# Kernel tuning notes

Hardware: AMD Instinct MI355X
Metric: run time of the kernel (lower is better)

The kernel has to match this reference:

```python
import jax, jax.numpy as jnp
import numpy as np

B, E, K = 2048, 16, 4
D_SF, D_OF, D_PPF, D_PVF = 512, 512, 256, 256
D = D_SF + D_OF + D_PPF + D_PVF  # 1536 = moe_input_size
H = 1024
N_OBJ, N_PRED = 36, 132
EPS = float(np.finfo(np.float64).eps)  # matches np.finfo(float).eps in combine
NOISE_EPS = 1e-2


def setup_inputs() -> dict:
    key = jax.random.key(0)
    ks = jax.random.split(key, 12)
    r = lambda i, shape, scale=1.0: (jax.random.normal(ks[i], shape, jnp.float32) * scale)
    return {
        "sf": r(0, (B, D_SF)),
        "of": r(1, (B, D_OF)),
        "ppf": r(2, (B, D_PPF)),
        "pvf": r(3, (B, D_PVF)),
        "w_gate": r(4, (D, E), 0.02),
        "w_noise": r(5, (D, E), 0.02),
        "W1": r(6, (E, D, H), 1.0 / np.sqrt(D)),
        "b1": jnp.zeros((E, H), jnp.float32),
        "W2": r(7, (E, H, H), 1.0 / np.sqrt(H)),
        "b2": jnp.zeros((E, H), jnp.float32),
        "Ws": r(8, (E, H, N_OBJ), 1.0 / np.sqrt(H)),
        "bs": jnp.zeros((E, N_OBJ), jnp.float32),
        "Wo": r(9, (E, H, N_OBJ), 1.0 / np.sqrt(H)),
        "bo": jnp.zeros((E, N_OBJ), jnp.float32),
        "Wp": r(10, (E, H, N_PRED), 1.0 / np.sqrt(H)),
        "bp": jnp.zeros((E, N_PRED), jnp.float32),
        "noise": r(11, (B, E)),
    }


def _noisy_top_k_gates(x, w_gate, w_noise, noise):
    """Shazeer noisy top-k gating -> sparse [B, E] gate matrix."""
    clean_logits = x @ w_gate                                   # [B, E]
    noise_stddev = jax.nn.softplus(x @ w_noise) + NOISE_EPS      # [B, E]
    logits = clean_logits + noise * noise_stddev
    top_vals, top_idx = jax.lax.top_k(logits, K)                 # [B, K]
    top_gates = jax.nn.softmax(top_vals, axis=-1)                # renormalized over top-k
    gates = jnp.zeros_like(logits)
    gates = gates.at[jnp.arange(x.shape[0])[:, None], top_idx].set(top_gates)
    return gates


def _combine(log_scores, gates):
    """SparseDispatcher.combine_expert_output, dense-equivalent.
    log_scores: [E, B, C] per-expert log-probs; gates: [B, E].
    output[b] = log(sum_e gates[b,e] * exp(log_scores[e,b])), eps where all-zero.
    gates==0 exactly zeroes the non-routed experts (same as sparse index_add).
    """
    w = gates.T[:, :, None]                                      # [E, B, 1]
    combined = jnp.sum(jnp.exp(log_scores) * w, axis=0)          # [B, C]
    combined = jnp.where(combined == 0, EPS, combined)
    return jnp.log(combined)


def reference(sf, of, ppf, pvf, w_gate, w_noise,
              W1, b1, W2, b2, Ws, bs, Wo, bo, Wp, bp, noise):
    x = jnp.concatenate([sf, of, ppf, pvf], axis=-1)             # [B, D]
    gates = _noisy_top_k_gates(x, w_gate, w_noise, noise)        # [B, E]

    # All-expert dense evaluation (grouped GEMM): 3-layer relu MLP trunk.
    h1 = jax.nn.relu(jnp.einsum('bd,edh->ebh', x, W1) + b1[:, None, :])   # [E, B, H]
    h2 = jax.nn.relu(jnp.einsum('ebh,ehg->ebg', h1, W2) + b2[:, None, :])  # [E, B, H]

    s_log = jax.nn.log_softmax(jnp.einsum('ebh,ehc->ebc', h2, Ws) + bs[:, None, :], axis=-1)
    o_log = jax.nn.log_softmax(jnp.einsum('ebh,ehc->ebc', h2, Wo) + bo[:, None, :], axis=-1)
    p_log = jax.nn.log_softmax(jnp.einsum('ebh,ehc->ebc', h2, Wp) + bp[:, None, :], axis=-1)

    s_out = _combine(s_log, gates)   # [B, N_OBJ]
    o_out = _combine(o_log, gates)   # [B, N_OBJ]
    p_out = _combine(p_log, gates)   # [B, N_PRED]
    return s_out, o_out, p_out
```

## Files before the change

kernel.cpp:

```cpp
#include <hip/hip_runtime.h>
#include <hip/hip_bf16.h>
#include <cstdint>

typedef __attribute__((ext_vector_type(8))) short short8;
typedef __attribute__((ext_vector_type(4))) float f32x4;

constexpr int B_ = 2048, E_ = 16, D_ = 1536, H_ = 1024;
constexpr int NHEAD = 256;
constexpr float EPS_ = 2.220446049250313e-16f;

__device__ __forceinline__ void gload_lds16(const void* g, void* l) {
  __builtin_amdgcn_global_load_lds((const __attribute__((address_space(1))) void*)g,
                                   (__attribute__((address_space(3))) void*)l,
                                   16, 0, 0);
}

__global__ __launch_bounds__(256) void pack_x(
    const float* __restrict__ sf, const float* __restrict__ of_,
    const float* __restrict__ ppf, const float* __restrict__ pvf,
    __hip_bfloat16* __restrict__ xb)
{
  const int b = blockIdx.x;
  for (int d = threadIdx.x; d < D_; d += 256) {
    float v;
    if (d < 512)       v = sf[b * 512 + d];
    else if (d < 1024) v = of_[b * 512 + (d - 512)];
    else if (d < 1280) v = ppf[b * 256 + (d - 1024)];
    else               v = pvf[b * 256 + (d - 1280)];
    xb[(size_t)b * D_ + d] = __float2bfloat16(v);
  }
}

__global__ __launch_bounds__(256) void gate_kernel(
    const float* __restrict__ sf, const float* __restrict__ of_,
    const float* __restrict__ ppf, const float* __restrict__ pvf,
    const float* __restrict__ wg, const float* __restrict__ wn,
    const float* __restrict__ noise,
    int* __restrict__ topidx, float* __restrict__ topw)
{
  __shared__ float xs[D_];
  __shared__ float sums[32];
  const int b = blockIdx.x, t = threadIdx.x;
  for (int d = t; d < D_; d += 256) {
    float v;
    if (d < 512)       v = sf[b * 512 + d];
    else if (d < 1024) v = of_[b * 512 + (d - 512)];
    else if (d < 1280) v = ppf[b * 256 + (d - 1024)];
    else               v = pvf[b * 256 + (d - 1280)];
    xs[d] = v;
  }
  __syncthreads();
  const int job = t >> 3, sub = t & 7;
  const int e = job & 15;
  const float* w = (job < 16) ? wg : wn;
  float p = 0.f;
  for (int d = sub; d < D_; d += 8) p += xs[d] * w[d * 16 + e];
  p += __shfl_down(p, 4, 8);
  p += __shfl_down(p, 2, 8);
  p += __shfl_down(p, 1, 8);
  if (sub == 0) sums[job] = p;
  __syncthreads();
  if (t == 0) {
    float lg[16];
    for (int i = 0; i < 16; ++i) {
      float z = sums[16 + i];
      float sp = (z > 0.f) ? (z + log1pf(expf(-z))) : log1pf(expf(z));
      lg[i] = sums[i] + noise[b * 16 + i] * (sp + 1e-2f);
    }
    float tv[4]; int ti[4];
    unsigned used = 0;
    for (int k = 0; k < 4; ++k) {
      float best = -INFINITY; int bi = 0;
      for (int i = 0; i < 16; ++i)
        if (!((used >> i) & 1u) && lg[i] > best) { best = lg[i]; bi = i; }
      used |= 1u << bi; tv[k] = best; ti[k] = bi;
    }
    float s = 0.f, ex[4];
    for (int k = 0; k < 4; ++k) { ex[k] = expf(tv[k] - tv[0]); s += ex[k]; }
    for (int k = 0; k < 4; ++k) { topw[b * 4 + k] = ex[k] / s; topidx[b * 4 + k] = ti[k]; }
  }
}

__global__ __launch_bounds__(256) void transpose_bf16(
    const float* __restrict__ src, __hip_bfloat16* __restrict__ dst, int K, int N)
{
  __shared__ float tile[32][33];
  const int e = blockIdx.z;
  const int n0 = blockIdx.x * 32, k0 = blockIdx.y * 32;
  const int tx = threadIdx.x, ty = threadIdx.y;
  const float* s = src + (size_t)e * K * N;
  __hip_bfloat16* d = dst + (size_t)e * N * K;
#pragma unroll
  for (int r = 0; r < 4; ++r) {
    const int k = k0 + ty + r * 8;
    tile[ty + r * 8][tx] = s[(size_t)k * N + n0 + tx];
  }
  __syncthreads();
#pragma unroll
  for (int r = 0; r < 4; ++r) {
    const int n = n0 + ty + r * 8;
    d[(size_t)n * K + k0 + tx] = __float2bfloat16(tile[tx][ty + r * 8]);
  }
}

__global__ __launch_bounds__(256) void head_transpose(
    const float* __restrict__ Wsp, const float* __restrict__ Wop,
    const float* __restrict__ Wpp, __hip_bfloat16* __restrict__ dst)
{
  __shared__ float tile[32][33];
  const int e = blockIdx.z;
  const int k0 = blockIdx.x * 32;
  const int n0 = blockIdx.y * 32;
  const int tx = threadIdx.x, ty = threadIdx.y;
#pragma unroll
  for (int r = 0; r < 4; ++r) {
    const int k = k0 + ty + r * 8;
    const int n = n0 + tx;
    float v;
    if (n < 36)       v = Wsp[((size_t)e * H_ + k) * 36 + n];
    else if (n < 72)  v = Wop[((size_t)e * H_ + k) * 36 + (n - 36)];
    else if (n < 204) v = Wpp[((size_t)e * H_ + k) * 132 + (n - 72)];
    else              v = 0.f;
    tile[ty + r * 8][tx] = v;
  }
  __syncthreads();
#pragma unroll
  for (int r = 0; r < 4; ++r) {
    const int n = n0 + ty + r * 8;
    dst[((size_t)e * NHEAD + n) * H_ + k0 + tx] = __float2bfloat16(tile[tx][ty + r * 8]);
  }
}

__global__ __launch_bounds__(256) void pack_hbias(
    const float* __restrict__ bs, const float* __restrict__ bo,
    const float* __restrict__ bp, float* __restrict__ hb)
{
  const int e = blockIdx.x, t = threadIdx.x;
  float v = 0.f;
  if (t < 36)       v = bs[e * 36 + t];
  else if (t < 72)  v = bo[e * 36 + (t - 36)];
  else if (t < 204) v = bp[e * 132 + (t - 72)];
  hb[e * NHEAD + t] = v;
}

template <int EPI>
__global__ __launch_bounds__(256) void gemm_bt(
    const __hip_bfloat16* __restrict__ A, size_t strideA, int ldA,
    const __hip_bfloat16* __restrict__ Bm, size_t strideB,
    const float* __restrict__ bias,
    void* __restrict__ Cout, size_t strideC, int ldC,
    int K)
{
  __shared__ __align__(16) __hip_bfloat16 lA[128 * 64];
  __shared__ __align__(16) __hip_bfloat16 lB[128 * 64];
  const int e = blockIdx.z;
  const int bm = blockIdx.x, bn = blockIdx.y;
  const int t = threadIdx.x;
  const int w = t >> 6, lane = t & 63;
  const int wm = w >> 1, wn = w & 1;
  const __hip_bfloat16* Ae = A + (size_t)e * strideA + (size_t)(bm * 128) * ldA;
  const __hip_bfloat16* Be = Bm + (size_t)e * strideB + (size_t)(bn * 128) * K;
  const int rsub = lane >> 3;
  const int csub = (lane & 7) * 8;

  f32x4 acc[4][4];
#pragma unroll
  for (int m = 0; m < 4; ++m)
#pragma unroll
    for (int n = 0; n < 4; ++n) acc[m][n] = (f32x4){0.f, 0.f, 0.f, 0.f};

  const int KT = K >> 6;
  const int arow = wm * 64 + (lane & 15);
  const int brow = wn * 64 + (lane & 15);
  const int khalf = (lane >> 4) * 8;

  for (int kt = 0; kt < KT; ++kt) {
    const int k0 = kt << 6;
    __syncthreads();
#pragma unroll
    for (int j = 0; j < 4; ++j) {
      const int r = j * 32 + w * 8 + rsub;
      gload_lds16(Ae + (size_t)r * ldA + (k0 + csub), &lA[j * 2048 + w * 512]);
      gload_lds16(Be + (size_t)r * K + (k0 + csub), &lB[j * 2048 + w * 512]);
    }
    asm volatile("s_waitcnt vmcnt(0)" ::: "memory");
    __syncthreads();
#pragma unroll
    for (int kk = 0; kk < 2; ++kk) {
      short8 af[4], bfr[4];
#pragma unroll
      for (int m = 0; m < 4; ++m)
        af[m] = *(const short8*)&lA[(arow + m * 16) * 64 + kk * 32 + khalf];
#pragma unroll
      for (int n = 0; n < 4; ++n)
        bfr[n] = *(const short8*)&lB[(brow + n * 16) * 64 + kk * 32 + khalf];
#pragma unroll
      for (int m = 0; m < 4; ++m)
#pragma unroll
        for (int n = 0; n < 4; ++n)
          acc[m][n] = __builtin_amdgcn_mfma_f32_16x16x32_bf16(af[m], bfr[n], acc[m][n], 0, 0, 0);
    }
  }

  const int rbase = (lane >> 4) * 4, cbase = lane & 15;
#pragma unroll
  for (int n = 0; n < 4; ++n) {
    const int gcol = bn * 128 + wn * 64 + n * 16 + cbase;
    const float bv = bias[(size_t)e * ldC + gcol];
#pragma unroll
    for (int m = 0; m < 4; ++m) {
      const int grow = bm * 128 + wm * 64 + m * 16 + rbase;
#pragma unroll
      for (int j = 0; j < 4; ++j) {
        float v = acc[m][n][j] + bv;
        const size_t idx = (size_t)e * strideC + (size_t)(grow + j) * ldC + gcol;
        if (EPI == 0) {
          ((__hip_bfloat16*)Cout)[idx] = __float2bfloat16(v > 0.f ? v : 0.f);
        } else {
          ((float*)Cout)[idx] = v;
        }
      }
    }
  }
}

__global__ __launch_bounds__(256) void combine_kernel(
    const float* __restrict__ logits, const int* __restrict__ topidx,
    const float* __restrict__ topw, float* __restrict__ out)
{
  __shared__ float rows[4][204];
  __shared__ float lse[4][3];
  __shared__ float wk[4];
  const int b = blockIdx.x, t = threadIdx.x;
  if (t < 4) wk[t] = topw[b * 4 + t];
#pragma unroll
  for (int k = 0; k < 4; ++k) {
    const int e = topidx[b * 4 + k];
    if (t < 204) rows[k][t] = logits[((size_t)e * B_ + b) * NHEAD + t];
  }
  __syncthreads();
  const int wv = t >> 6, lane = t & 63;
  const int segbase[3] = {0, 36, 72};
  const int segcnt[3] = {36, 36, 132};
  for (int s = 0; s < 3; ++s) {
    float mx = -INFINITY;
    for (int c = lane; c < segcnt[s]; c += 64) mx = fmaxf(mx, rows[wv][segbase[s] + c]);
    for (int o = 32; o > 0; o >>= 1) mx = fmaxf(mx, __shfl_xor(mx, o));
    float sum = 0.f;
    for (int c = lane; c < segcnt[s]; c += 64) sum += expf(rows[wv][segbase[s] + c] - mx);
    for (int o = 32; o > 0; o >>= 1) sum += __shfl_xor(sum, o);
    if (lane == 0) lse[wv][s] = mx + logf(sum);
  }
  __syncthreads();
  if (t < 204) {
    const int seg = t < 36 ? 0 : (t < 72 ? 1 : 2);
    float acc = 0.f;
    for (int k = 0; k < 4; ++k) acc += wk[k] * expf(rows[k][t] - lse[k][seg]);
    if (acc == 0.f) acc = EPS_;
    const float r = logf(acc);
    if (t < 36)      out[b * 36 + t] = r;
    else if (t < 72) out[73728 + b * 36 + (t - 36)] = r;
    else             out[147456 + b * 132 + (t - 72)] = r;
  }
}

extern "C" void kernel_launch(void* const* d_in, const int* in_sizes, int n_in,
                              void* d_out, int out_size, void* d_ws, size_t ws_size,
                              hipStream_t stream)
{
  (void)in_sizes; (void)n_in; (void)out_size; (void)ws_size;
  const float* sf      = (const float*)d_in[0];
  const float* of_     = (const float*)d_in[1];
  const float* ppf     = (const float*)d_in[2];
  const float* pvf     = (const float*)d_in[3];
  const float* w_gate  = (const float*)d_in[4];
  const float* w_noise = (const float*)d_in[5];
  const float* W1      = (const float*)d_in[6];
  const float* b1      = (const float*)d_in[7];
  const float* W2      = (const float*)d_in[8];
  const float* b2      = (const float*)d_in[9];
  const float* Ws      = (const float*)d_in[10];
  const float* bs      = (const float*)d_in[11];
  const float* Wo      = (const float*)d_in[12];
  const float* bo      = (const float*)d_in[13];
  const float* Wp      = (const float*)d_in[14];
  const float* bp      = (const float*)d_in[15];
  const float* noise   = (const float*)d_in[16];

  char* ws = (char*)d_ws;
  size_t off = 0;
  auto take = [&](size_t bytes) -> void* {
    void* p = ws + off; off += (bytes + 255) & ~(size_t)255; return p;
  };
  __hip_bfloat16* xb  = (__hip_bfloat16*)take((size_t)B_ * D_ * 2);
  __hip_bfloat16* W1T = (__hip_bfloat16*)take((size_t)E_ * H_ * D_ * 2);
  __hip_bfloat16* W2T = (__hip_bfloat16*)take((size_t)E_ * H_ * H_ * 2);
  __hip_bfloat16* WhT = (__hip_bfloat16*)take((size_t)E_ * NHEAD * H_ * 2);
  float* hbias        = (float*)take((size_t)E_ * NHEAD * 4);
  __hip_bfloat16* h1  = (__hip_bfloat16*)take((size_t)E_ * B_ * H_ * 2);
  __hip_bfloat16* h2  = (__hip_bfloat16*)take((size_t)E_ * B_ * H_ * 2);
  int* topidx         = (int*)take((size_t)B_ * 4 * 4);
  float* topw         = (float*)take((size_t)B_ * 4 * 4);
  float* logits       = (float*)h1;

  pack_x<<<B_, 256, 0, stream>>>(sf, of_, ppf, pvf, xb);
  gate_kernel<<<B_, 256, 0, stream>>>(sf, of_, ppf, pvf, w_gate, w_noise, noise, topidx, topw);
  transpose_bf16<<<dim3(H_ / 32, D_ / 32, E_), dim3(32, 8), 0, stream>>>(W1, W1T, D_, H_);
  transpose_bf16<<<dim3(H_ / 32, H_ / 32, E_), dim3(32, 8), 0, stream>>>(W2, W2T, H_, H_);
  head_transpose<<<dim3(H_ / 32, NHEAD / 32, E_), dim3(32, 8), 0, stream>>>(Ws, Wo, Wp, WhT);
  pack_hbias<<<E_, 256, 0, stream>>>(bs, bo, bp, hbias);

  gemm_bt<0><<<dim3(B_ / 128, H_ / 128, E_), 256, 0, stream>>>(
      xb, 0, D_, W1T, (size_t)H_ * D_, b1, h1, (size_t)B_ * H_, H_, D_);
  gemm_bt<0><<<dim3(B_ / 128, H_ / 128, E_), 256, 0, stream>>>(
      h1, (size_t)B_ * H_, H_, W2T, (size_t)H_ * H_, b2, h2, (size_t)B_ * H_, H_, H_);
  gemm_bt<1><<<dim3(B_ / 128, NHEAD / 128, E_), 256, 0, stream>>>(
      h2, (size_t)B_ * H_, H_, WhT, (size_t)NHEAD * H_, hbias, logits, (size_t)B_ * NHEAD, NHEAD, H_);

  combine_kernel<<<B_, 256, 0, stream>>>(logits, topidx, topw, (float*)d_out);
}
```

Baseline: 661.0 us.

## Route tokens to top-k experts and run sparse grouped GEMMs

Replaces dense all-expert evaluation with MoE-style routing. The gate kernel counts tokens per expert, a schedule kernel builds per-expert 128-row tiles, rows are gathered into a packed buffer, and the three GEMMs run only over routed rows via a tile table. This cuts GEMM work to the top-4 of 16 experts. In exchange it adds several small serial kernels and atomics, and it caps the schedule at 80 tiles, which could drop rows if the expert distribution is skewed.

```diff
diff --git a/kernel.cpp b/kernel.cpp
--- a/kernel.cpp
+++ b/kernel.cpp
@@ -7,6 +7,8 @@
 
 constexpr int B_ = 2048, E_ = 16, D_ = 1536, H_ = 1024;
 constexpr int NHEAD = 256;
+constexpr int TOTROWS = B_ * 4;
+constexpr int MAXTILES = 80;
 constexpr float EPS_ = 2.220446049250313e-16f;
 
 __device__ __forceinline__ void gload_lds16(const void* g, void* l) {
@@ -15,20 +17,8 @@
                                    16, 0, 0);
 }
 
-__global__ __launch_bounds__(256) void pack_x(
-    const float* __restrict__ sf, const float* __restrict__ of_,
-    const float* __restrict__ ppf, const float* __restrict__ pvf,
-    __hip_bfloat16* __restrict__ xb)
-{
-  const int b = blockIdx.x;
-  for (int d = threadIdx.x; d < D_; d += 256) {
-    float v;
-    if (d < 512)       v = sf[b * 512 + d];
-    else if (d < 1024) v = of_[b * 512 + (d - 512)];
-    else if (d < 1280) v = ppf[b * 256 + (d - 1024)];
-    else               v = pvf[b * 256 + (d - 1280)];
-    xb[(size_t)b * D_ + d] = __float2bfloat16(v);
-  }
+__global__ __launch_bounds__(64) void zero_small(int* __restrict__ p, int n) {
+  if ((int)threadIdx.x < n) p[threadIdx.x] = 0;
 }
 
 __global__ __launch_bounds__(256) void gate_kernel(
@@ -36,7 +26,7 @@
     const float* __restrict__ ppf, const float* __restrict__ pvf,
     const float* __restrict__ wg, const float* __restrict__ wn,
     const float* __restrict__ noise,
-    int* __restrict__ topidx, float* __restrict__ topw)
+    int* __restrict__ topidx, float* __restrict__ topw, int* __restrict__ counts)
 {
   __shared__ float xs[D_];
   __shared__ float sums[32];
@@ -77,7 +67,69 @@
     }
     float s = 0.f, ex[4];
     for (int k = 0; k < 4; ++k) { ex[k] = expf(tv[k] - tv[0]); s += ex[k]; }
-    for (int k = 0; k < 4; ++k) { topw[b * 4 + k] = ex[k] / s; topidx[b * 4 + k] = ti[k]; }
+    for (int k = 0; k < 4; ++k) {
+      topw[b * 4 + k] = ex[k] / s; topidx[b * 4 + k] = ti[k];
+      atomicAdd(&counts[ti[k]], 1);
+    }
+  }
+}
+
+__global__ __launch_bounds__(64) void schedule_kernel(
+    const int* __restrict__ counts, int* __restrict__ offsets, int* __restrict__ ntiles,
+    int* __restrict__ tile_e, int* __restrict__ tile_rb, int* __restrict__ tile_len)
+{
+  if (threadIdx.x != 0) return;
+  int off = 0, nt = 0;
+  for (int e = 0; e < E_; ++e) {
+    offsets[e] = off;
+    int c = counts[e];
+    if (c < 0) c = 0;
+    if (c > TOTROWS) c = TOTROWS;
+    for (int m0 = 0; m0 < c && nt < MAXTILES; m0 += 128) {
+      tile_e[nt] = e; tile_rb[nt] = off + m0;
+      tile_len[nt] = (c - m0 < 128) ? (c - m0) : 128;
+      ++nt;
+    }
+    off += c;
+  }
+  offsets[E_] = off;
+  *ntiles = nt;
+}
+
+__global__ __launch_bounds__(256) void build_rows(
+    const int* __restrict__ topidx, const int* __restrict__ offsets,
+    int* __restrict__ cursor, int* __restrict__ rowtok, int* __restrict__ slot)
+{
+  const int b = blockIdx.x * 256 + threadIdx.x;
+  if (b >= B_) return;
+#pragma unroll
+  for (int k = 0; k < 4; ++k) {
+    const int e = topidx[b * 4 + k];
+    const int p = atomicAdd(&cursor[e], 1);
+    int row = offsets[e] + p;
+    if (row < 0) row = 0;
+    if (row >= TOTROWS) row = TOTROWS - 1;
+    rowtok[row] = b;
+    slot[b * 4 + k] = row;
+  }
+}
+
+__global__ __launch_bounds__(256) void gather_x(
+    const float* __restrict__ sf, const float* __restrict__ of_,
+    const float* __restrict__ ppf, const float* __restrict__ pvf,
+    const int* __restrict__ rowtok, __hip_bfloat16* __restrict__ xp)
+{
+  const int row = blockIdx.x;
+  int b = rowtok[row];
+  if (b < 0) b = 0;
+  if (b >= B_) b = B_ - 1;
+  for (int d = threadIdx.x; d < D_; d += 256) {
+    float v;
+    if (d < 512)       v = sf[b * 512 + d];
+    else if (d < 1024) v = of_[b * 512 + (d - 512)];
+    else if (d < 1280) v = ppf[b * 256 + (d - 1024)];
+    else               v = pvf[b * 256 + (d - 1280)];
+    xp[(size_t)row * D_ + d] = __float2bfloat16(v);
   }
 }
 
@@ -144,24 +196,38 @@
 }
 
 template <int EPI>
-__global__ __launch_bounds__(256) void gemm_bt(
-    const __hip_bfloat16* __restrict__ A, size_t strideA, int ldA,
+__global__ __launch_bounds__(256) void gemm_sp(
+    const int* __restrict__ ntiles, const int* __restrict__ tile_e,
+    const int* __restrict__ tile_rb, const int* __restrict__ tile_len,
+    const __hip_bfloat16* __restrict__ Ap, int ldA,
     const __hip_bfloat16* __restrict__ Bm, size_t strideB,
     const float* __restrict__ bias,
-    void* __restrict__ Cout, size_t strideC, int ldC,
-    int K)
+    void* __restrict__ Cout, int ldC, int K)
 {
   __shared__ __align__(16) __hip_bfloat16 lA[128 * 64];
   __shared__ __align__(16) __hip_bfloat16 lB[128 * 64];
-  const int e = blockIdx.z;
-  const int bm = blockIdx.x, bn = blockIdx.y;
+  const int ti = blockIdx.x;
+  int nt = *ntiles;
+  if (nt > MAXTILES) nt = MAXTILES;
+  if (ti >= nt) return;
+  const int e = tile_e[ti] & 15, rb = tile_rb[ti], L = tile_len[ti];
+  const int bn = blockIdx.y;
   const int t = threadIdx.x;
   const int w = t >> 6, lane = t & 63;
   const int wm = w >> 1, wn = w & 1;
-  const __hip_bfloat16* Ae = A + (size_t)e * strideA + (size_t)(bm * 128) * ldA;
   const __hip_bfloat16* Be = Bm + (size_t)e * strideB + (size_t)(bn * 128) * K;
   const int rsub = lane >> 3;
   const int csub = (lane & 7) * 8;
+
+  int arows[4];
+#pragma unroll
+  for (int j = 0; j < 4; ++j) {
+    int rloc = j * 32 + w * 8 + rsub;
+    int r = rb + (rloc < L ? rloc : L - 1);
+    if (r < 0) r = 0;
+    if (r >= TOTROWS) r = TOTROWS - 1;
+    arows[j] = r;
+  }
 
   f32x4 acc[4][4];
 #pragma unroll
@@ -180,7 +246,7 @@
 #pragma unroll
     for (int j = 0; j < 4; ++j) {
       const int r = j * 32 + w * 8 + rsub;
-      gload_lds16(Ae + (size_t)r * ldA + (k0 + csub), &lA[j * 2048 + w * 512]);
+      gload_lds16(Ap + (size_t)arows[j] * ldA + (k0 + csub), &lA[j * 2048 + w * 512]);
       gload_lds16(Be + (size_t)r * K + (k0 + csub), &lB[j * 2048 + w * 512]);
     }
     asm volatile("s_waitcnt vmcnt(0)" ::: "memory");
@@ -209,15 +275,18 @@
     const float bv = bias[(size_t)e * ldC + gcol];
 #pragma unroll
     for (int m = 0; m < 4; ++m) {
-      const int grow = bm * 128 + wm * 64 + m * 16 + rbase;
+      const int rloc0 = wm * 64 + m * 16 + rbase;
 #pragma unroll
       for (int j = 0; j < 4; ++j) {
-        float v = acc[m][n][j] + bv;
-        const size_t idx = (size_t)e * strideC + (size_t)(grow + j) * ldC + gcol;
-        if (EPI == 0) {
-          ((__hip_bfloat16*)Cout)[idx] = __float2bfloat16(v > 0.f ? v : 0.f);
-        } else {
-          ((float*)Cout)[idx] = v;
+        const int rloc = rloc0 + j;
+        if (rloc < L && rb + rloc < TOTROWS) {
+          float v = acc[m][n][j] + bv;
+          const size_t idx = (size_t)(rb + rloc) * ldC + gcol;
+          if (EPI == 0) {
+            ((__hip_bfloat16*)Cout)[idx] = __float2bfloat16(v > 0.f ? v : 0.f);
+          } else {
+            ((float*)Cout)[idx] = v;
+          }
         }
       }
     }
@@ -225,7 +294,7 @@
 }
 
 __global__ __launch_bounds__(256) void combine_kernel(
-    const float* __restrict__ logits, const int* __restrict__ topidx,
+    const float* __restrict__ logits, const int* __restrict__ slot,
     const float* __restrict__ topw, float* __restrict__ out)
 {
   __shared__ float rows[4][204];
@@ -235,8 +304,10 @@
   if (t < 4) wk[t] = topw[b * 4 + t];
 #pragma unroll
   for (int k = 0; k < 4; ++k) {
-    const int e = topidx[b * 4 + k];
-    if (t < 204) rows[k][t] = logits[((size_t)e * B_ + b) * NHEAD + t];
+    int row = slot[b * 4 + k];
+    if (row < 0) row = 0;
+    if (row >= TOTROWS) row = TOTROWS - 1;
+    if (t < 204) rows[k][t] = logits[(size_t)row * NHEAD + t];
   }
   __syncthreads();
   const int wv = t >> 6, lane = t & 63;
@@ -292,30 +363,45 @@
   auto take = [&](size_t bytes) -> void* {
     void* p = ws + off; off += (bytes + 255) & ~(size_t)255; return p;
   };
-  __hip_bfloat16* xb  = (__hip_bfloat16*)take((size_t)B_ * D_ * 2);
   __hip_bfloat16* W1T = (__hip_bfloat16*)take((size_t)E_ * H_ * D_ * 2);
   __hip_bfloat16* W2T = (__hip_bfloat16*)take((size_t)E_ * H_ * H_ * 2);
   __hip_bfloat16* WhT = (__hip_bfloat16*)take((size_t)E_ * NHEAD * H_ * 2);
   float* hbias        = (float*)take((size_t)E_ * NHEAD * 4);
-  __hip_bfloat16* h1  = (__hip_bfloat16*)take((size_t)E_ * B_ * H_ * 2);
-  __hip_bfloat16* h2  = (__hip_bfloat16*)take((size_t)E_ * B_ * H_ * 2);
+  __hip_bfloat16* xp  = (__hip_bfloat16*)take((size_t)TOTROWS * D_ * 2);
+  __hip_bfloat16* h1p = (__hip_bfloat16*)take((size_t)TOTROWS * H_ * 2);
+  __hip_bfloat16* h2p = (__hip_bfloat16*)take((size_t)TOTROWS * H_ * 2);
+  float* logitsp      = (float*)take((size_t)TOTROWS * NHEAD * 4);
+  int* counts         = (int*)take(64 * 4);
+  int* cursor         = (int*)take(64 * 4);
+  int* offsets        = (int*)take(64 * 4);
+  int* ntiles         = (int*)take(64 * 4);
+  int* tile_e         = (int*)take(MAXTILES * 4);
+  int* tile_rb        = (int*)take(MAXTILES * 4);
+  int* tile_len       = (int*)take(MAXTILES * 4);
   int* topidx         = (int*)take((size_t)B_ * 4 * 4);
   float* topw         = (float*)take((size_t)B_ * 4 * 4);
-  float* logits       = (float*)h1;
-
-  pack_x<<<B_, 256, 0, stream>>>(sf, of_, ppf, pvf, xb);
-  gate_kernel<<<B_, 256, 0, stream>>>(sf, of_, ppf, pvf, w_gate, w_noise, noise, topidx, topw);
+  int* rowtok         = (int*)take((size_t)TOTROWS * 4);
+  int* slot           = (int*)take((size_t)B_ * 4 * 4);
+
+  zero_small<<<1, 64, 0, stream>>>(counts, E_);
+  zero_small<<<1, 64, 0, stream>>>(cursor, E_);
+  gate_kernel<<<B_, 256, 0, stream>>>(sf, of_, ppf, pvf, w_gate, w_noise, noise,
+                                      topidx, topw, counts);
+  schedule_kernel<<<1, 64, 0, stream>>>(counts, offsets, ntiles, tile_e, tile_rb, tile_len);
+  build_rows<<<(B_ + 255) / 256, 256, 0, stream>>>(topidx, offsets, cursor, rowtok, slot);
+  gather_x<<<TOTROWS, 256, 0, stream>>>(sf, of_, ppf, pvf, rowtok, xp);
+
   transpose_bf16<<<dim3(H_ / 32, D_ / 32, E_), dim3(32, 8), 0, stream>>>(W1, W1T, D_, H_);
   transpose_bf16<<<dim3(H_ / 32, H_ / 32, E_), dim3(32, 8), 0, stream>>>(W2, W2T, H_, H_);
   head_transpose<<<dim3(H_ / 32, NHEAD / 32, E_), dim3(32, 8), 0, stream>>>(Ws, Wo, Wp, WhT);
   pack_hbias<<<E_, 256, 0, stream>>>(bs, bo, bp, hbias);
 
-  gemm_bt<0><<<dim3(B_ / 128, H_ / 128, E_), 256, 0, stream>>>(
-      xb, 0, D_, W1T, (size_t)H_ * D_, b1, h1, (size_t)B_ * H_, H_, D_);
-  gemm_bt<0><<<dim3(B_ / 128, H_ / 128, E_), 256, 0, stream>>>(
-      h1, (size_t)B_ * H_, H_, W2T, (size_t)H_ * H_, b2, h2, (size_t)B_ * H_, H_, H_);
-  gemm_bt<1><<<dim3(B_ / 128, NHEAD / 128, E_), 256, 0, stream>>>(
-      h2, (size_t)B_ * H_, H_, WhT, (size_t)NHEAD * H_, hbias, logits, (size_t)B_ * NHEAD, NHEAD, H_);
-
-  combine_kernel<<<B_, 256, 0, stream>>>(logits, topidx, topw, (float*)d_out);
-}
+  gemm_sp<0><<<dim3(MAXTILES, H_ / 128), 256, 0, stream>>>(
+      ntiles, tile_e, tile_rb, tile_len, xp, D_, W1T, (size_t)H_ * D_, b1, h1p, H_, D_);
+  gemm_sp<0><<<dim3(MAXTILES, H_ / 128), 256, 0, stream>>>(
+      ntiles, tile_e, tile_rb, tile_len, h1p, H_, W2T, (size_t)H_ * H_, b2, h2p, H_, H_);
+  gemm_sp<1><<<dim3(MAXTILES, NHEAD / 128), 256, 0, stream>>>(
+      ntiles, tile_e, tile_rb, tile_len, h2p, H_, WhT, (size_t)NHEAD * H_, hbias, logitsp, NHEAD, H_);
+
+  combine_kernel<<<B_, 256, 0, stream>>>(logitsp, slot, topw, (float*)d_out);
+}
```

Result: slower. 692.1 us (+4.7%).
